# Optimization experiments

Hardware: AMD Instinct MI355X
Metric: run time of the kernel (lower is better)

Reference implementation:

```python
import jax, jax.numpy as jnp
import numpy as np

N_HEAD = 8

def setup_inputs() -> dict:
    key = jax.random.key(0)
    ks = jax.random.split(key, 5)
    N, C, T, V = 64, 128, 64, 25
    x = jax.random.normal(ks[0], (N, C, T, V), dtype=jnp.float32)
    Wa = jax.random.normal(ks[1], (C, C), dtype=jnp.float32) * (1.0 / np.sqrt(C))
    ba = jax.random.normal(ks[2], (C,), dtype=jnp.float32) * 0.01
    Wp = jax.random.normal(ks[3], (C, C), dtype=jnp.float32) * (1.0 / np.sqrt(C))
    bp = jax.random.normal(ks[4], (C,), dtype=jnp.float32) * 0.01
    temp = jnp.ones((N_HEAD, 1), dtype=jnp.float32)
    denom_bias = jnp.zeros((N_HEAD, 1, 1), dtype=jnp.float32)
    return {"x": x, "Wa": Wa, "ba": ba, "Wp": Wp, "bp": bp, "temp": temp, "denom_bias": denom_bias}

def reference(x, Wa, ba, Wp, bp, temp, denom_bias):
    # x: (N, C, T, V); eval mode (dropout = identity); residual = identity (in==out, stride==1)
    N, C, T, V = x.shape
    H = N_HEAD
    hd = C // H
    res = x
    # 1x1 conv c_attn
    w = jnp.einsum('nctv,oc->notv', x, Wa) + ba[None, :, None, None]
    # (N,H,hd,T,V) -> (N,H,T,V,hd) -> (N,H,T*V,hd)
    w = w.reshape(N, H, hd, T, V).transpose(0, 1, 3, 4, 2).reshape(N, H, T * V, hd)
    w_sq = w * w
    denom = jnp.maximum(jnp.cumsum(w_sq, axis=2), 1e-12)
    w_normed = w_sq / denom + denom_bias  # denom_bias (H,1,1) broadcasts
    tmp = jnp.sum(w_normed, axis=-1) * temp  # (N,H,L) * (H,1)
    Pi = jax.nn.softmax(tmp, axis=2)  # (N,H,L)
    dots = jnp.cumsum(w_sq * Pi[..., None], axis=2) / (jnp.cumsum(Pi, axis=2) + 1e-8)[..., None]
    attn = 1.0 / (1.0 + dots)
    y = -(w * Pi[..., None]) * attn  # (N,H,L,hd)
    y = y.reshape(N, H, T, V, hd).transpose(0, 1, 4, 2, 3).reshape(N, C, T, V)
    y = jnp.einsum('nctv,oc->notv', y, Wp) + bp[None, :, None, None]
    y = y + res
    return jax.nn.relu(y)
```

## Files before the change

### kernel.cpp

```cpp
#include <hip/hip_runtime.h>
#include <hip/hip_bf16.h>

#define N_S     64
#define C_CH    128
#define L_SEQ   1600
#define H_HEADS 8
#define HD      16
#define SEGN    32
#define SEGL    50
#define PADW    136
#define PADT    72
#define SLABD   804

typedef __attribute__((ext_vector_type(8))) short bf16x8;
typedef __attribute__((ext_vector_type(4))) float f32x4;

__device__ inline unsigned short f2bf(float f) {
  return __builtin_bit_cast(unsigned short, __float2bfloat16(f));
}
__device__ inline float bflo(unsigned int u) { return __builtin_bit_cast(float, u << 16); }
__device__ inline float bfhi(unsigned int u) { return __builtin_bit_cast(float, u & 0xffff0000u); }
__device__ inline unsigned int pk(float a, float b) {
  return (unsigned int)f2bf(a) | ((unsigned int)f2bf(b) << 16);
}

template <int CTRL>
__device__ inline float dppadd(float x) {
  int r = __builtin_amdgcn_update_dpp(0, __builtin_bit_cast(int, x), CTRL, 0xF, 0xF, true);
  return x + __builtin_bit_cast(float, r);
}

__global__ __launch_bounds__(256) void k_gemm1(const float* __restrict__ x,
                                               const float* __restrict__ Wa,
                                               const float* __restrict__ ba,
                                               unsigned short* __restrict__ w2) {
  __shared__ unsigned short was[128 * PADW];
  __shared__ unsigned short xs[128 * PADT];
  const int n = blockIdx.y;
  const int l0 = blockIdx.x * 64;
  const int t = threadIdx.x;
  const float* xn = x + (size_t)n * (C_CH * L_SEQ);

#pragma unroll
  for (int it = 0; it < 16; ++it) {
    int pos = it * 256 + t;
    int o = pos >> 5;
    int c4 = (pos & 31) << 2;
    float4 v = *reinterpret_cast<const float4*>(Wa + o * C_CH + c4);
    ushort4 u;
    u.x = f2bf(v.x); u.y = f2bf(v.y); u.z = f2bf(v.z); u.w = f2bf(v.w);
    *reinterpret_cast<ushort4*>(&was[o * PADW + c4]) = u;
  }
#pragma unroll
  for (int it = 0; it < 8; ++it) {
    int pos = it * 256 + t;
    int c = pos >> 4;
    int l4 = (pos & 15) << 2;
    float4 v = *reinterpret_cast<const float4*>(xn + (size_t)c * L_SEQ + l0 + l4);
    ushort4 u;
    u.x = f2bf(v.x); u.y = f2bf(v.y); u.z = f2bf(v.z); u.w = f2bf(v.w);
    *reinterpret_cast<ushort4*>(&xs[c * PADT + l4]) = u;
  }
  __syncthreads();

  const int wv = t >> 6;
  const int lane = t & 63;
  const int r16 = lane & 15;
  const int kg = lane >> 4;
  f32x4 acc[8];
#pragma unroll
  for (int ot = 0; ot < 8; ++ot) acc[ot] = (f32x4){0.f, 0.f, 0.f, 0.f};

#pragma unroll
  for (int ks = 0; ks < 4; ++ks) {
    bf16x8 a;
#pragma unroll
    for (int j = 0; j < 8; ++j)
      a[j] = (short)xs[(ks * 32 + kg * 8 + j) * PADT + wv * 16 + r16];
#pragma unroll
    for (int ot = 0; ot < 8; ++ot) {
      bf16x8 b = *reinterpret_cast<const bf16x8*>(&was[(ot * 16 + r16) * PADW + ks * 32 + kg * 8]);
      acc[ot] = __builtin_amdgcn_mfma_f32_16x16x32_bf16(a, b, acc[ot], 0, 0, 0);
    }
  }
  __syncthreads();
#pragma unroll
  for (int ot = 0; ot < 8; ++ot) {
    float bav = ba[ot * 16 + r16];
    ushort4 u;
    u.x = f2bf(acc[ot][0] + bav);
    u.y = f2bf(acc[ot][1] + bav);
    u.z = f2bf(acc[ot][2] + bav);
    u.w = f2bf(acc[ot][3] + bav);
    *reinterpret_cast<ushort4*>(&xs[(ot * 16 + r16) * PADT + wv * 16 + kg * 4]) = u;
  }
  __syncthreads();
#pragma unroll
  for (int it = 0; it < 4; ++it) {
    int pos = it * 256 + t;
    int c = pos >> 3;
    int l8 = (pos & 7) << 3;
    uint4 vv = *reinterpret_cast<const uint4*>(&xs[c * PADT + l8]);
    *reinterpret_cast<uint4*>(w2 + ((size_t)n * C_CH + c) * L_SEQ + l0 + l8) = vv;
  }
}

__global__ __launch_bounds__(512, 4) void k_scan(const unsigned short* __restrict__ w2,
                                                 unsigned short* __restrict__ y2,
                                                 const float* __restrict__ temp,
                                                 const float* __restrict__ dbias) {
  __shared__ float slab[16 * SLABD];
  __shared__ float stot[SEGN][17];
  __shared__ float red[8];

  const int nh = blockIdx.x;
  const int h = nh & 7;
  const int t = threadIdx.x;
  const int d = t & 15;
  const int lane = t & 63;
  const int wv = t >> 6;
  const int seg = t >> 4;
  const float tscale = temp[h];
  const float db16 = 16.f * dbias[h];
  const float M = fmaxf((16.f + db16) * tscale, db16 * tscale);

  const unsigned short* srcg = w2 + (size_t)nh * (HD * L_SEQ);
#pragma unroll
  for (int it = 0; it < 7; ++it) {
    int q = it * 512 + t;
    if (q < 3200) {
      uint4 vq = *reinterpret_cast<const uint4*>(srcg + (size_t)q * 8);
      int row = q / 200;
      int colq = q - row * 200;
      *reinterpret_cast<uint4*>(&slab[row * SLABD + colq * 4]) = vq;
    }
  }
  __syncthreads();

  unsigned int vp[25];
  const int rb = d * SLABD + seg * 25;
#pragma unroll
  for (int ii = 0; ii < 25; ++ii)
    vp[ii] = __builtin_bit_cast(unsigned int, slab[rb + ii]);

  float tot = 0.f;
#pragma unroll
  for (int ii = 0; ii < 25; ++ii) {
    float a = bflo(vp[ii]), b = bfhi(vp[ii]);
    tot += a * a + b * b;
  }
  stot[seg][d] = tot;
  __syncthreads();
#pragma unroll
  for (int it = 0; it < 2; ++it) {
    int col = wv + it * 8;
    float val = (lane < 32) ? stot[lane][col] : 0.f;
#pragma unroll
    for (int sh = 1; sh < 32; sh <<= 1) {
      float nv = __shfl_up(val, sh);
      if (lane >= sh) val += nv;
    }
    if (lane < 32) stot[lane][col] = val;
  }
  __syncthreads();
  const float off = stot[seg][d] - tot;

  unsigned int ep[25];
  float run = off;
  float sAcc = 0.f, wpAcc = 0.f;
  float eprev = 0.f;
#pragma unroll
  for (int i = 0; i < SEGL; ++i) {
    float v = (i & 1) ? bfhi(vp[i >> 1]) : bflo(vp[i >> 1]);
    float wsq = v * v;
    run += wsq;
    float c = __fdividef(wsq, fmaxf(run, 1e-12f));
    c = dppadd<0x128>(c);
    c = dppadd<0x124>(c);
    c = dppadd<0x122>(c);
    c = dppadd<0x121>(c);
    float e = __expf((c + db16) * tscale - M);
    sAcc += e;
    wpAcc = fmaf(wsq, e, wpAcc);
    if (i & 1) ep[i >> 1] = pk(eprev, e); else eprev = e;
  }
  {
    float s = sAcc;
#pragma unroll
    for (int mask = 32; mask; mask >>= 1) s += __shfl_xor(s, mask);
    if (lane == 0) red[wv] = s;
  }
  __syncthreads();
  float S16 = 0.f;
#pragma unroll
  for (int i2 = 0; i2 < 8; ++i2) S16 += red[i2];
  const float S = S16 * 0.0625f;
  const float ninvS = -1.0f / S;
  const float epsS = 1e-8f * S;

  stot[seg][d] = wpAcc;
  if (d == 0) stot[seg][16] = sAcc;
  __syncthreads();
#pragma unroll
  for (int it = 0; it < 2; ++it) {
    int col = wv + it * 8;
    float val = (lane < 32) ? stot[lane][col] : 0.f;
#pragma unroll
    for (int sh = 1; sh < 32; sh <<= 1) {
      float nv = __shfl_up(val, sh);
      if (lane >= sh) val += nv;
    }
    if (lane < 32) stot[lane][col] = val;
  }
  if (wv == 0) {
    float val = (lane < 32) ? stot[lane][16] : 0.f;
#pragma unroll
    for (int sh = 1; sh < 32; sh <<= 1) {
      float nv = __shfl_up(val, sh);
      if (lane >= sh) val += nv;
    }
    if (lane < 32) stot[lane][16] = val;
  }
  __syncthreads();
  const float wp_off = stot[seg][d] - wpAcc;
  const float pi_off = stot[seg][16] - sAcc;

  {
    float run_wp = wp_off, run_pi = pi_off;
    float ylo = 0.f;
#pragma unroll
    for (int i = 0; i < SEGL; ++i) {
      float v = (i & 1) ? bfhi(vp[i >> 1]) : bflo(vp[i >> 1]);
      float e = (i & 1) ? bfhi(ep[i >> 1]) : bflo(ep[i >> 1]);
      run_pi += e;
      run_wp = fmaf(v * v, e, run_wp);
      float dn = run_pi + epsS;
      float y = (v * e) * __fdividef(dn, dn + run_wp) * ninvS;
      if (i & 1) vp[i >> 1] = pk(ylo, y); else ylo = y;
    }
  }

#pragma unroll
  for (int ii = 0; ii < 25; ++ii)
    slab[rb + ii] = __builtin_bit_cast(float, vp[ii]);
  __syncthreads();
  unsigned short* dstg = y2 + (size_t)nh * (HD * L_SEQ);
#pragma unroll
  for (int it = 0; it < 7; ++it) {
    int q = it * 512 + t;
    if (q < 3200) {
      int row = q / 200;
      int colq = q - row * 200;
      uint4 vq = *reinterpret_cast<const uint4*>(&slab[row * SLABD + colq * 4]);
      *reinterpret_cast<uint4*>(dstg + (size_t)q * 8) = vq;
    }
  }
}

__global__ __launch_bounds__(256) void k_gemm2(const unsigned short* __restrict__ y2,
                                               const float* __restrict__ Wp,
                                               const float* __restrict__ bp,
                                               const float* __restrict__ x,
                                               float* __restrict__ out) {
  __shared__ unsigned short wps[128 * PADW];
  __shared__ unsigned short ys[128 * PADT];
  const int n = blockIdx.y;
  const int l0 = blockIdx.x * 64;
  const int t = threadIdx.x;

#pragma unroll
  for (int it = 0; it < 16; ++it) {
    int pos = it * 256 + t;
    int o = pos >> 5;
    int c4 = (pos & 31) << 2;
    float4 v = *reinterpret_cast<const float4*>(Wp + o * C_CH + c4);
    ushort4 u;
    u.x = f2bf(v.x); u.y = f2bf(v.y); u.z = f2bf(v.z); u.w = f2bf(v.w);
    *reinterpret_cast<ushort4*>(&wps[o * PADW + c4]) = u;
  }
#pragma unroll
  for (int it = 0; it < 4; ++it) {
    int pos = it * 256 + t;
    int c = pos >> 3;
    int l8 = (pos & 7) << 3;
    uint4 v = *reinterpret_cast<const uint4*>(y2 + ((size_t)n * C_CH + c) * L_SEQ + l0 + l8);
    *reinterpret_cast<uint4*>(&ys[c * PADT + l8]) = v;
  }
  __syncthreads();

  const int wv = t >> 6;
  const int lane = t & 63;
  const int r16 = lane & 15;
  const int kg = lane >> 4;
  f32x4 acc[8];
#pragma unroll
  for (int ot = 0; ot < 8; ++ot) acc[ot] = (f32x4){0.f, 0.f, 0.f, 0.f};

#pragma unroll
  for (int ks = 0; ks < 4; ++ks) {
    bf16x8 b;
#pragma unroll
    for (int j = 0; j < 8; ++j)
      b[j] = (short)ys[(ks * 32 + kg * 8 + j) * PADT + wv * 16 + r16];
#pragma unroll
    for (int ot = 0; ot < 8; ++ot) {
      bf16x8 a = *reinterpret_cast<const bf16x8*>(&wps[(ot * 16 + r16) * PADW + ks * 32 + kg * 8]);
      acc[ot] = __builtin_amdgcn_mfma_f32_16x16x32_bf16(a, b, acc[ot], 0, 0, 0);
    }
  }
  const int gl = l0 + wv * 16 + r16;
#pragma unroll
  for (int ot = 0; ot < 8; ++ot) {
#pragma unroll
    for (int i = 0; i < 4; ++i) {
      int o = ot * 16 + kg * 4 + i;
      size_t idx = (size_t)n * (C_CH * L_SEQ) + (size_t)o * L_SEQ + gl;
      float r = acc[ot][i] + bp[o] + x[idx];
      out[idx] = fmaxf(r, 0.f);
    }
  }
}

extern "C" void kernel_launch(void* const* d_in, const int* in_sizes, int n_in,
                              void* d_out, int out_size, void* d_ws, size_t ws_size,
                              hipStream_t stream) {
  const float* x     = (const float*)d_in[0];
  const float* Wa    = (const float*)d_in[1];
  const float* ba    = (const float*)d_in[2];
  const float* Wp    = (const float*)d_in[3];
  const float* bp    = (const float*)d_in[4];
  const float* temp  = (const float*)d_in[5];
  const float* dbias = (const float*)d_in[6];
  float* out = (float*)d_out;

  unsigned short* w2 = (unsigned short*)d_ws;
  unsigned short* y2 = w2 + (size_t)N_S * H_HEADS * L_SEQ * HD;

  k_gemm1<<<dim3(L_SEQ / 64, N_S), 256, 0, stream>>>(x, Wa, ba, w2);
  k_scan<<<N_S * H_HEADS, 512, 0, stream>>>(w2, y2, temp, dbias);
  k_gemm2<<<dim3(L_SEQ / 64, N_S), 256, 0, stream>>>(y2, Wp, bp, x, out);
}
```

Baseline: 81.75 us.

## Restructure scan kernel so each thread owns all 16 head dims for 4 positions

```diff
diff --git a/kernel.cpp b/kernel.cpp
--- a/kernel.cpp
+++ b/kernel.cpp
@@ -6,11 +6,8 @@
 #define L_SEQ   1600
 #define H_HEADS 8
 #define HD      16
-#define SEGN    32
-#define SEGL    50
 #define PADW    136
 #define PADT    72
-#define SLABD   804
 
 typedef __attribute__((ext_vector_type(8))) short bf16x8;
 typedef __attribute__((ext_vector_type(4))) float f32x4;
@@ -22,12 +19,6 @@
 __device__ inline float bfhi(unsigned int u) { return __builtin_bit_cast(float, u & 0xffff0000u); }
 __device__ inline unsigned int pk(float a, float b) {
   return (unsigned int)f2bf(a) | ((unsigned int)f2bf(b) << 16);
-}
-
-template <int CTRL>
-__device__ inline float dppadd(float x) {
-  int r = __builtin_amdgcn_update_dpp(0, __builtin_bit_cast(int, x), CTRL, 0xF, 0xF, true);
-  return x + __builtin_bit_cast(float, r);
 }
 
 __global__ __launch_bounds__(256) void k_gemm1(const float* __restrict__ x,
@@ -105,155 +96,198 @@
   }
 }
 
-__global__ __launch_bounds__(512, 4) void k_scan(const unsigned short* __restrict__ w2,
-                                                 unsigned short* __restrict__ y2,
-                                                 const float* __restrict__ temp,
-                                                 const float* __restrict__ dbias) {
-  __shared__ float slab[16 * SLABD];
-  __shared__ float stot[SEGN][17];
+__global__ __launch_bounds__(512) void k_scan(const unsigned short* __restrict__ w2,
+                                              unsigned short* __restrict__ y2,
+                                              const float* __restrict__ temp,
+                                              const float* __restrict__ dbias) {
+  __shared__ unsigned int sl[13600];
   __shared__ float red[8];
+  float* stotf = (float*)sl;
 
   const int nh = blockIdx.x;
   const int h = nh & 7;
   const int t = threadIdx.x;
-  const int d = t & 15;
   const int lane = t & 63;
   const int wv = t >> 6;
-  const int seg = t >> 4;
+  const bool act = (t < 400);
   const float tscale = temp[h];
   const float db16 = 16.f * dbias[h];
   const float M = fmaxf((16.f + db16) * tscale, db16 * tscale);
-
-  const unsigned short* srcg = w2 + (size_t)nh * (HD * L_SEQ);
-#pragma unroll
-  for (int it = 0; it < 7; ++it) {
-    int q = it * 512 + t;
-    if (q < 3200) {
-      uint4 vq = *reinterpret_cast<const uint4*>(srcg + (size_t)q * 8);
-      int row = q / 200;
-      int colq = q - row * 200;
-      *reinterpret_cast<uint4*>(&slab[row * SLABD + colq * 4]) = vq;
-    }
-  }
-  __syncthreads();
-
-  unsigned int vp[25];
-  const int rb = d * SLABD + seg * 25;
-#pragma unroll
-  for (int ii = 0; ii < 25; ++ii)
-    vp[ii] = __builtin_bit_cast(unsigned int, slab[rb + ii]);
-
-  float tot = 0.f;
-#pragma unroll
-  for (int ii = 0; ii < 25; ++ii) {
-    float a = bflo(vp[ii]), b = bfhi(vp[ii]);
-    tot += a * a + b * b;
-  }
-  stot[seg][d] = tot;
-  __syncthreads();
-#pragma unroll
-  for (int it = 0; it < 2; ++it) {
-    int col = wv + it * 8;
-    float val = (lane < 32) ? stot[lane][col] : 0.f;
-#pragma unroll
-    for (int sh = 1; sh < 32; sh <<= 1) {
-      float nv = __shfl_up(val, sh);
-      if (lane >= sh) val += nv;
-    }
-    if (lane < 32) stot[lane][col] = val;
-  }
-  __syncthreads();
-  const float off = stot[seg][d] - tot;
-
-  unsigned int ep[25];
-  float run = off;
-  float sAcc = 0.f, wpAcc = 0.f;
-  float eprev = 0.f;
-#pragma unroll
-  for (int i = 0; i < SEGL; ++i) {
-    float v = (i & 1) ? bfhi(vp[i >> 1]) : bflo(vp[i >> 1]);
-    float wsq = v * v;
-    run += wsq;
-    float c = __fdividef(wsq, fmaxf(run, 1e-12f));
-    c = dppadd<0x128>(c);
-    c = dppadd<0x124>(c);
-    c = dppadd<0x122>(c);
-    c = dppadd<0x121>(c);
-    float e = __expf((c + db16) * tscale - M);
-    sAcc += e;
-    wpAcc = fmaf(wsq, e, wpAcc);
-    if (i & 1) ep[i >> 1] = pk(eprev, e); else eprev = e;
-  }
+  const float A = tscale * 1.44269504088896f;
+  const float B = (db16 * tscale - M) * 1.44269504088896f;
+
+  const unsigned int* srcd = reinterpret_cast<const unsigned int*>(w2) + (size_t)nh * 12800;
+#pragma unroll
+  for (int dd = 0; dd < 16; ++dd) {
+    sl[t * 17 + dd] = srcd[dd * 800 + t];
+    if (t < 288) sl[(512 + t) * 17 + dd] = srcd[dd * 800 + 512 + t];
+  }
+  __syncthreads();
+
+  unsigned int vpA[16], vpB[16];
+  if (act) {
+#pragma unroll
+    for (int dd = 0; dd < 16; ++dd) {
+      vpA[dd] = sl[(2 * t) * 17 + dd];
+      vpB[dd] = sl[(2 * t + 1) * 17 + dd];
+    }
+  }
+
+  float run[16];
+  if (act) {
+#pragma unroll
+    for (int dd = 0; dd < 16; ++dd) {
+      float a0 = bflo(vpA[dd]), a1 = bfhi(vpA[dd]);
+      float b0 = bflo(vpB[dd]), b1 = bfhi(vpB[dd]);
+      run[dd] = a0 * a0 + a1 * a1 + b0 * b0 + b1 * b1;
+    }
+  }
+  __syncthreads();
+  if (act) {
+#pragma unroll
+    for (int dd = 0; dd < 16; ++dd) stotf[t * 17 + dd] = run[dd];
+  }
+  __syncthreads();
+
   {
-    float s = sAcc;
+#pragma unroll
+    for (int cc = 0; cc < 2; ++cc) {
+      int col = wv + cc * 8;
+      float carry = 0.f;
+#pragma unroll
+      for (int ch = 0; ch < 7; ++ch) {
+        int idx = ch * 64 + lane;
+        bool a2 = idx < 400;
+        float val = a2 ? stotf[idx * 17 + col] : 0.f;
+#pragma unroll
+        for (int sh = 1; sh < 64; sh <<= 1) {
+          float nv = __shfl_up(val, sh);
+          if (lane >= sh) val += nv;
+        }
+        val += carry;
+        if (a2) stotf[idx * 17 + col] = val;
+        carry = __shfl(val, 63);
+      }
+    }
+  }
+  __syncthreads();
+  if (act) {
+#pragma unroll
+    for (int dd = 0; dd < 16; ++dd) run[dd] = stotf[t * 17 + dd] - run[dd];
+  }
+
+  float wpt[16], wsqs[16], e0v, e1v, e2v, e3v;
+  float sAcc = 0.f;
+  if (act) {
+#pragma unroll
+    for (int dd = 0; dd < 16; ++dd) wpt[dd] = 0.f;
+#define LSTEP(VP, HI, EV)                                              \
+    {                                                                  \
+      float c = 0.f;                                                   \
+      _Pragma("unroll")                                                \
+      for (int dd = 0; dd < 16; ++dd) {                                \
+        float v = HI ? bfhi(VP[dd]) : bflo(VP[dd]);                    \
+        float wsq = v * v;                                             \
+        wsqs[dd] = wsq;                                                \
+        run[dd] += wsq;                                                \
+        c += wsq * __frcp_rn(fmaxf(run[dd], 1e-12f));                  \
+      }                                                                \
+      EV = exp2f(fmaf(c, A, B));                                       \
+      sAcc += EV;                                                      \
+      _Pragma("unroll")                                                \
+      for (int dd = 0; dd < 16; ++dd) wpt[dd] = fmaf(wsqs[dd], EV, wpt[dd]); \
+    }
+    LSTEP(vpA, 0, e0v)
+    LSTEP(vpA, 1, e1v)
+    LSTEP(vpB, 0, e2v)
+    LSTEP(vpB, 1, e3v)
+#undef LSTEP
+  }
+  {
+    float s = act ? sAcc : 0.f;
 #pragma unroll
     for (int mask = 32; mask; mask >>= 1) s += __shfl_xor(s, mask);
     if (lane == 0) red[wv] = s;
   }
   __syncthreads();
-  float S16 = 0.f;
-#pragma unroll
-  for (int i2 = 0; i2 < 8; ++i2) S16 += red[i2];
-  const float S = S16 * 0.0625f;
+  float S = 0.f;
+#pragma unroll
+  for (int i2 = 0; i2 < 8; ++i2) S += red[i2];
   const float ninvS = -1.0f / S;
   const float epsS = 1e-8f * S;
 
-  stot[seg][d] = wpAcc;
-  if (d == 0) stot[seg][16] = sAcc;
-  __syncthreads();
-#pragma unroll
-  for (int it = 0; it < 2; ++it) {
-    int col = wv + it * 8;
-    float val = (lane < 32) ? stot[lane][col] : 0.f;
-#pragma unroll
-    for (int sh = 1; sh < 32; sh <<= 1) {
-      float nv = __shfl_up(val, sh);
-      if (lane >= sh) val += nv;
-    }
-    if (lane < 32) stot[lane][col] = val;
-  }
-  if (wv == 0) {
-    float val = (lane < 32) ? stot[lane][16] : 0.f;
-#pragma unroll
-    for (int sh = 1; sh < 32; sh <<= 1) {
-      float nv = __shfl_up(val, sh);
-      if (lane >= sh) val += nv;
-    }
-    if (lane < 32) stot[lane][16] = val;
-  }
-  __syncthreads();
-  const float wp_off = stot[seg][d] - wpAcc;
-  const float pi_off = stot[seg][16] - sAcc;
-
+  if (act) {
+#pragma unroll
+    for (int dd = 0; dd < 16; ++dd) stotf[t * 17 + dd] = wpt[dd];
+    stotf[t * 17 + 16] = sAcc;
+  }
+  __syncthreads();
   {
-    float run_wp = wp_off, run_pi = pi_off;
-    float ylo = 0.f;
-#pragma unroll
-    for (int i = 0; i < SEGL; ++i) {
-      float v = (i & 1) ? bfhi(vp[i >> 1]) : bflo(vp[i >> 1]);
-      float e = (i & 1) ? bfhi(ep[i >> 1]) : bflo(ep[i >> 1]);
-      run_pi += e;
-      run_wp = fmaf(v * v, e, run_wp);
-      float dn = run_pi + epsS;
-      float y = (v * e) * __fdividef(dn, dn + run_wp) * ninvS;
-      if (i & 1) vp[i >> 1] = pk(ylo, y); else ylo = y;
-    }
-  }
-
-#pragma unroll
-  for (int ii = 0; ii < 25; ++ii)
-    slab[rb + ii] = __builtin_bit_cast(float, vp[ii]);
-  __syncthreads();
-  unsigned short* dstg = y2 + (size_t)nh * (HD * L_SEQ);
-#pragma unroll
-  for (int it = 0; it < 7; ++it) {
-    int q = it * 512 + t;
-    if (q < 3200) {
-      int row = q / 200;
-      int colq = q - row * 200;
-      uint4 vq = *reinterpret_cast<const uint4*>(&slab[row * SLABD + colq * 4]);
-      *reinterpret_cast<uint4*>(dstg + (size_t)q * 8) = vq;
-    }
+    int ncols = (wv == 0) ? 3 : 2;
+    for (int cc = 0; cc < ncols; ++cc) {
+      int col = (cc < 2) ? (wv + cc * 8) : 16;
+      float carry = 0.f;
+#pragma unroll
+      for (int ch = 0; ch < 7; ++ch) {
+        int idx = ch * 64 + lane;
+        bool a2 = idx < 400;
+        float val = a2 ? stotf[idx * 17 + col] : 0.f;
+#pragma unroll
+        for (int sh = 1; sh < 64; sh <<= 1) {
+          float nv = __shfl_up(val, sh);
+          if (lane >= sh) val += nv;
+        }
+        val += carry;
+        if (a2) stotf[idx * 17 + col] = val;
+        carry = __shfl(val, 63);
+      }
+    }
+  }
+  __syncthreads();
+  float run_pi = 0.f;
+  if (act) {
+#pragma unroll
+    for (int dd = 0; dd < 16; ++dd) run[dd] = stotf[t * 17 + dd] - wpt[dd];
+    run_pi = stotf[t * 17 + 16] - sAcc;
+  }
+
+  if (act) {
+#define YSTEP(VP, HI, EV, STORE_LO, STORE_HI)                          \
+    {                                                                  \
+      run_pi += EV;                                                    \
+      float dn = run_pi + epsS;                                        \
+      float g = EV * ninvS;                                            \
+      _Pragma("unroll")                                                \
+      for (int dd = 0; dd < 16; ++dd) {                                \
+        float v = HI ? bfhi(VP[dd]) : bflo(VP[dd]);                    \
+        run[dd] = fmaf(v * v, EV, run[dd]);                            \
+        float attn = dn * __frcp_rn(dn + run[dd]);                     \
+        float y = v * g * attn;                                        \
+        if (STORE_LO) wsqs[dd] = y;                                    \
+        if (STORE_HI) VP[dd] = pk(wsqs[dd], y);                        \
+      }                                                                \
+    }
+    YSTEP(vpA, 0, e0v, 1, 0)
+    YSTEP(vpA, 1, e1v, 0, 1)
+    YSTEP(vpB, 0, e2v, 1, 0)
+    YSTEP(vpB, 1, e3v, 0, 1)
+#undef YSTEP
+  }
+
+  __syncthreads();
+  if (act) {
+#pragma unroll
+    for (int dd = 0; dd < 16; ++dd) {
+      sl[(2 * t) * 17 + dd] = vpA[dd];
+      sl[(2 * t + 1) * 17 + dd] = vpB[dd];
+    }
+  }
+  __syncthreads();
+  unsigned int* dstd = reinterpret_cast<unsigned int*>(y2) + (size_t)nh * 12800;
+#pragma unroll
+  for (int dd = 0; dd < 16; ++dd) {
+    dstd[dd * 800 + t] = sl[t * 17 + dd];
+    if (t < 288) dstd[dd * 800 + 512 + t] = sl[(512 + t) * 17 + dd];
   }
 }
 
```

Result: slower. 96.21 us (+17.7%).
